# Kernel tuning notes

Measured on AMD Instinct MI355X. Metric: run time of the kernel, lower is better.

Reference implementation:

```python
import jax, jax.numpy as jnp
import numpy as np

EPS = 1e-5

def masked_group_norm(x, mask, gamma, beta, num_groups):
    # x: [B,D,H,W,C] (zero at unoccupied), mask: [B,D,H,W,1] float
    B, D, H, W, C = x.shape
    G = num_groups
    Cg = C // G
    xg = x.reshape(B, -1, G, Cg)          # [B,V,G,Cg]
    m = mask.reshape(B, -1, 1, 1)         # [B,V,1,1]
    cnt = jnp.maximum(m.sum(axis=1, keepdims=True) * Cg, 1.0)  # elems per (B,G)
    mean = (xg * m).sum(axis=(1, 3), keepdims=True) / cnt
    var = (((xg - mean) ** 2) * m).sum(axis=(1, 3), keepdims=True) / cnt
    y = (xg - mean) * jax.lax.rsqrt(var + EPS)
    y = y.reshape(B, D, H, W, C)
    return (y * gamma + beta) * mask

def downsample2(x, mask):
    # mean-pool occupied children under coords//2; new site occupied if any child is
    B, D, H, W, C = x.shape
    xr = x.reshape(B, D // 2, 2, H // 2, 2, W // 2, 2, C)
    mr = mask.reshape(B, D // 2, 2, H // 2, 2, W // 2, 2, 1)
    cnt = mr.sum(axis=(2, 4, 6))
    y = xr.sum(axis=(2, 4, 6)) / jnp.maximum(cnt, 1.0)
    new_mask = (cnt > 0).astype(x.dtype)
    return y, new_mask

def subm_conv3d(x, w, b, mask):
    # submanifold conv: unoccupied inputs are zero; outputs only at occupied sites
    y = jax.lax.conv_general_dilated(
        x, w, window_strides=(1, 1, 1), padding='SAME',
        dimension_numbers=('NDHWC', 'DHWIO', 'NDHWC'))
    return (y + b) * mask

def setup_inputs() -> dict:
    key = jax.random.key(0)
    ks = jax.random.split(key, 12)
    B, D, C, Co = 4, 64, 64, 128
    x = jax.random.normal(ks[0], (B, D, D, D, C), dtype=jnp.float32)
    mask = jax.random.randint(ks[1], (B, D, D, D), 0, 2).astype(jnp.int32)
    s = 0.05
    return {
        'x': x, 'mask': mask,
        'gn1_w': jnp.ones((C,), jnp.float32), 'gn1_b': jnp.zeros((C,), jnp.float32),
        'w1': jax.random.normal(ks[2], (3, 3, 3, C, Co), jnp.float32) * s,
        'b1': jax.random.normal(ks[3], (Co,), jnp.float32) * s,
        'gn2_w': jnp.ones((Co,), jnp.float32), 'gn2_b': jnp.zeros((Co,), jnp.float32),
        'w2': jax.random.normal(ks[4], (3, 3, 3, Co, Co), jnp.float32) * s,
        'b2': jax.random.normal(ks[5], (Co,), jnp.float32) * s,
        'wskip': jax.random.normal(ks[6], (C, Co), jnp.float32) * s,
        'bskip': jax.random.normal(ks[7], (Co,), jnp.float32) * s,
    }

def reference(x, mask, gn1_w, gn1_b, w1, b1, gn2_w, gn2_b, w2, b2, wskip, bskip):
    NUM_GROUPS = 32
    m = mask.astype(x.dtype)[..., None]          # [B,D,H,W,1]
    x = x * m                                    # sparse tensor: zero off-mask
    # act_layers: SparseGroupNorm32 + SparseSiLU
    h = masked_group_norm(x, m, gn1_w, gn1_b, NUM_GROUPS)
    h = jax.nn.silu(h)                           # silu(0)=0, stays sparse
    # downsample both h and residual x
    h, dm = downsample2(h, m)
    xd, _ = downsample2(x, m)
    # out_layers: conv3 -> GN -> SiLU -> conv3
    h = subm_conv3d(h, w1, b1, dm)
    h = masked_group_norm(h, dm, gn2_w, gn2_b, NUM_GROUPS)
    h = jax.nn.silu(h)
    h = subm_conv3d(h, w2, b2, dm)
    # skip: 1x1 sparse conv (out_channels != channels)
    skip = (jnp.einsum('bdhwc,co->bdhwo', xd, wskip) + bskip) * dm
    return h + skip
```

## Files before the change

kernel.cpp:

```cpp
#include <hip/hip_runtime.h>
#include <cstdint>
#include <cstddef>

#define B_ 4
#define V1 262144
#define C1 64
#define V2 32768
#define C2 128
#define TOTV 131072
#define P_ 34
#define P2_ 1156
#define P3_ 39304
#define SBSTRIDE ((size_t)4 * P3_)

#define OFF_S1A 0
#define OFF_S2A 128
#define OFF_CNT1 256
#define OFF_S1B 260
#define OFF_S2B 388
#define OFF_CNT2 516

typedef __bf16 bf16x8 __attribute__((ext_vector_type(8)));
typedef float f32x4 __attribute__((ext_vector_type(4)));

__device__ __forceinline__ float bf2f(unsigned short u) {
    return __builtin_bit_cast(float, (unsigned)u << 16);
}
__device__ __forceinline__ unsigned short f2bf(float f) {
    unsigned u = __builtin_bit_cast(unsigned, f);
    u += 0x7fffu + ((u >> 16) & 1u);
    return (unsigned short)(u >> 16);
}
__device__ __forceinline__ float fast_silu(float x) {
    return x * __builtin_amdgcn_rcpf(1.f + __expf(-x));
}

__device__ __forceinline__ int a_ofs(int ks, int csh) {
    int s = ks & ((1 << csh) - 1), tap = ks >> csh;
    int dz = tap / 9, r = tap % 9, dy = r / 3, dx = r % 3;
    return s * (int)(SBSTRIDE * 64) + (dz * P2_ + dy * P_ + dx) * 64;
}

__global__ __launch_bounds__(256) void k0z_prep(const float* __restrict__ w1,
                                                const float* __restrict__ w2,
                                                const float* __restrict__ wskip,
                                                unsigned short* __restrict__ w1t,
                                                unsigned short* __restrict__ w2t,
                                                int* __restrict__ d1,
                                                int* __restrict__ d2,
                                                unsigned short* __restrict__ h1p,
                                                unsigned short* __restrict__ h2p)
{
    if (blockIdx.x >= 2624) {
        int i = (blockIdx.x - 2624) * 256 + threadIdx.x;
        if (i >= 24 * P3_) return;
        int sb = i / P3_, vox = i % P3_;
        int vz = vox / P2_, r = vox % P2_, vy = r / P_, vx = r % P_;
        bool border = (vz == 0) | (vz == 33) | (vy == 0) | (vy == 33) | (vx == 0) | (vx == 33);
        if (!border) return;
        unsigned short* base = (sb < 8) ? (h1p + (size_t)sb * P3_ * 32 + (size_t)vox * 32)
                                        : (h2p + (size_t)(sb - 8) * P3_ * 32 + (size_t)vox * 32);
        uint4 z = {0, 0, 0, 0};
        uint4* b4 = (uint4*)base;
        b4[0] = z; b4[1] = z; b4[2] = z; b4[3] = z;
        return;
    }
    int i = blockIdx.x * 256 + threadIdx.x;
    if (blockIdx.x == 0) {
        int t = threadIdx.x;
        if (t < 54)               d1[t] = (t + 1 < 54)  ? a_ofs(t + 1, 1) - a_ofs(t, 1) : 0;
        if (t >= 64 && t < 172) { int j = t - 64;
                                  d2[j] = (j + 1 < 108) ? a_ofs(j + 1, 2) - a_ofs(j, 2) : 0; }
    }
    if (i < 54 * 4096) {
        int slab = i >> 12, r = i & 4095;
        int q = r >> 10, n = (r >> 3) & 127, j = r & 7;
        int t = slab >> 1, s = slab & 1;
        int ci = s * 32 + q * 8 + j;
        w1t[i] = f2bf(w1[((size_t)t * 64 + ci) * 128 + n]);
    }
    int i2 = i - 54 * 4096;
    if (i2 >= 0 && i2 < 110 * 4096) {
        int slab = i2 >> 12, r = i2 & 4095;
        int q = r >> 10, n = (r >> 3) & 127, j = r & 7;
        float v;
        if (slab < 108) {
            int t = slab >> 2, s = slab & 3;
            int ci = s * 32 + q * 8 + j;
            v = w2[((size_t)t * 128 + ci) * 128 + n];
        } else {
            int ci = (slab - 108) * 32 + q * 8 + j;
            v = wskip[(size_t)ci * 128 + n];
        }
        w2t[i2] = f2bf(v);
    }
}

__global__ __launch_bounds__(256) void k1_stats1(const float* __restrict__ x,
                                                 const int* __restrict__ mask,
                                                 float* __restrict__ stats)
{
    __shared__ float ls1[32], ls2[32];
    __shared__ float lcnt;
    int tid = threadIdx.x;
    if (tid < 32) { ls1[tid] = 0.f; ls2[tid] = 0.f; }
    if (tid == 0) lcnt = 0.f;
    __syncthreads();

    int b  = blockIdx.x & 3;
    int bb = blockIdx.x >> 2;
    int c4 = tid & 15;
    int vl = tid >> 4;

    const float* xb = x + ((size_t)b * V1) * C1;
    const int*   mb = mask + (size_t)b * V1;

    float s1a = 0.f, s2a = 0.f, s1b = 0.f, s2b = 0.f, mc = 0.f;
    for (int ch = bb; ch < V1 / 16; ch += 1024) {
        int v = ch * 16 + vl;
        int m = mb[v];
        if (c4 == 0) mc += (float)m;
        if (m) {
            float4 xv = *(const float4*)(xb + (size_t)v * C1 + c4 * 4);
            s1a += xv.x + xv.y;  s2a += xv.x * xv.x + xv.y * xv.y;
            s1b += xv.z + xv.w;  s2b += xv.z * xv.z + xv.w * xv.w;
        }
    }
    atomicAdd(&ls1[2 * c4],     s1a); atomicAdd(&ls2[2 * c4],     s2a);
    atomicAdd(&ls1[2 * c4 + 1], s1b); atomicAdd(&ls2[2 * c4 + 1], s2b);
    if (c4 == 0) atomicAdd(&lcnt, mc);
    __syncthreads();
    if (tid < 32) {
        atomicAdd(&stats[OFF_S1A + b * 32 + tid], ls1[tid]);
        atomicAdd(&stats[OFF_S2A + b * 32 + tid], ls2[tid]);
    }
    if (tid == 0) atomicAdd(&stats[OFF_CNT1 + b], lcnt);
}

__global__ __launch_bounds__(256) void k2_down(const float* __restrict__ x,
                                               const int* __restrict__ mask,
                                               const float* __restrict__ gn1w,
                                               const float* __restrict__ gn1b,
                                               float* __restrict__ stats,
                                               unsigned short* __restrict__ h1p,
                                               unsigned short* __restrict__ xdb,
                                               float* __restrict__ dm)
{
    __shared__ float bcnt;
    int tid = threadIdx.x;
    if (tid == 0) bcnt = 0.f;
    __syncthreads();
    int c  = tid & 63;
    int vl = tid >> 6;
    const size_t ovbase = (size_t)blockIdx.x * 32;
    const int b = (int)(ovbase >> 15);

    int g = c >> 1;
    float ce   = fmaxf(stats[OFF_CNT1 + b] * 2.f, 1.f);
    float mean = stats[OFF_S1A + b * 32 + g] / ce;
    float var  = stats[OFF_S2A + b * 32 + g] / ce - mean * mean;
    float rinv = rsqrtf(var + 1e-5f);
    float a  = rinv * gn1w[c];
    float bc = gn1b[c] - mean * a;

    const int*   mb = mask + ((size_t)b << 18);
    const float* xb = x + (((size_t)b << 18) << 6);

    float mycnt = 0.f;
    #pragma unroll 2
    for (int it = 0; it < 8; ++it) {
        size_t ov = ovbase + it * 4 + vl;
        int v2 = (int)(ov & 32767);
        int z = v2 >> 10, y = (v2 >> 5) & 31, xk = v2 & 31;

        float hacc = 0.f, xacc = 0.f; int cnt = 0;
        #pragma unroll
        for (int dz = 0; dz < 2; ++dz)
        #pragma unroll
        for (int dy = 0; dy < 2; ++dy)
        #pragma unroll
        for (int dx = 0; dx < 2; ++dx) {
            int v1 = ((2 * z + dz) << 12) | ((2 * y + dy) << 6) | (2 * xk + dx);
            if (mb[v1]) {
                cnt++;
                float xv = xb[(size_t)v1 * 64 + c];
                xacc += xv;
                hacc += fast_silu(fmaf(xv, a, bc));
            }
        }
        float inv = __builtin_amdgcn_rcpf(fmaxf((float)cnt, 1.f));
        int pvox = (z + 1) * P2_ + (y + 1) * P_ + (xk + 1);
        size_t so = ((size_t)(c >> 5) * SBSTRIDE + (size_t)b * P3_ + pvox) * 32 + (c & 31);
        h1p[so] = f2bf(hacc * inv);
        xdb[ov * 64 + c] = f2bf(xacc * inv);
        if (c == 0) {
            float d = (cnt > 0) ? 1.f : 0.f;
            dm[ov] = d;
            mycnt += d;
        }
    }
    if (c == 0) atomicAdd(&bcnt, mycnt);
    __syncthreads();
    if (tid == 0) atomicAdd(&stats[OFF_CNT2 + b], bcnt);
}

template<int CIN, bool SKIP>
__global__ __launch_bounds__(256, 2) void conv3_mfma(
    const unsigned short* __restrict__ srcP,
    const unsigned short* __restrict__ sksrc,
    const unsigned short* __restrict__ wT,
    const int* __restrict__ tblA,
    const float* __restrict__ bias,
    const float* __restrict__ bias2,
    const float* __restrict__ dm,
    float* __restrict__ outf,
    unsigned short* __restrict__ outb,
    float* __restrict__ statsOut)
{
    constexpr int CS   = CIN / 32;
    constexpr int NKM  = 27 * CS;
    constexpr int NPHM = NKM / 2;
    constexpr int NPH  = NPHM + (SKIP ? 1 : 0);

    __shared__ short smem[2][8192];

    const int tid  = threadIdx.x;
    const int lane = tid & 63;
    const int wv   = tid >> 6;
    const int orig = blockIdx.x;
    const int blk  = (orig & 7) * 64 + (orig >> 3);
    const int b    = blk >> 7;
    const int z    = (blk >> 2) & 31;
    const int yo   = blk & 3;
    const int y0   = yo * 8 + wv * 2;
    const int vb   = b * 32768;
    const int klo  = (lane >> 4) * 8;
    const int xl   = lane & 15;
    const int rlo  = (lane >> 4) * 4;

    f32x4 acc[4][8];
    #pragma unroll
    for (int f = 0; f < 4; ++f)
        #pragma unroll
        for (int nb = 0; nb < 8; ++nb)
            acc[f][nb] = (f32x4){0.f, 0.f, 0.f, 0.f};

    const char* pA = (const char*)srcP +
        (((size_t)b * P3_ + (size_t)(z * P2_ + y0 * P_ + xl)) * 32 + klo) * 2;

    auto loadSkip = [&](int ss, bf16x8* af) {
        const unsigned short* abase = sksrc + ss * 32;
        #pragma unroll
        for (int fy = 0; fy < 2; ++fy)
            #pragma unroll
            for (int fx = 0; fx < 2; ++fx)
                af[fy * 2 + fx] = *(const bf16x8*)(abase +
                    (size_t)(vb + z * 1024 + (y0 + fy) * 32 + fx * 16 + xl) * 64 + klo);
    };

    auto stageW = [&](int pr, int buf) {
        const char* g = (const char*)wT + (size_t)pr * 16384 + wv * 1024 + (lane << 4);
        char* l = (char*)&smem[0][0] + buf * 16384 + wv * 1024;
        #pragma unroll
        for (int j = 0; j < 4; ++j)
            __builtin_amdgcn_global_load_lds(
                (const __attribute__((address_space(1))) unsigned int*)(g + j * 4096),
                (__attribute__((address_space(3))) unsigned int*)(l + j * 4096),
                16, 0, 0);
    };

    auto loadAStep = [&](int ks, bf16x8* af) {
        af[0] = *(const bf16x8*)pA;
        af[1] = *(const bf16x8*)(pA + 1024);
        af[2] = *(const bf16x8*)(pA + 2176);
        af[3] = *(const bf16x8*)(pA + 3200);
        pA += tblA[ks];
    };

    bf16x8 afc[8];
    stageW(0, 0);
    loadAStep(0, &afc[0]);
    loadAStep(1, &afc[4]);
    asm volatile("s_waitcnt vmcnt(8)" ::: "memory");
    __builtin_amdgcn_s_barrier();

    int cur = 0;
    #pragma unroll 2
    for (int p = 0; p < NPH; ++p) {
        const bool more = (p + 1 < NPH);
        bf16x8 afn[8] = {{}, {}, {}, {}, {}, {}, {}, {}};
        if (more) {
            stageW(p + 1, cur ^ 1);
            if (2 * p + 2 < NKM) {
                loadAStep(2 * p + 2, &afn[0]);
                loadAStep(2 * p + 3, &afn[4]);
            } else if (SKIP) {
                loadSkip(0, &afn[0]);
                loadSkip(1, &afn[4]);
            }
        }
        __builtin_amdgcn_s_setprio(1);
        #pragma unroll
        for (int ss = 0; ss < 2; ++ss) {
            const short* bp = &smem[0][0] + cur * 8192 + ss * 4096 +
                              ((lane >> 4) * 128 + xl) * 8;
            #pragma unroll
            for (int nb = 0; nb < 8; ++nb) {
                bf16x8 bfr = *(const bf16x8*)(bp + nb * 128);
                acc[0][nb] = __builtin_amdgcn_mfma_f32_16x16x32_bf16(afc[ss * 4 + 0], bfr, acc[0][nb], 0, 0, 0);
                acc[1][nb] = __builtin_amdgcn_mfma_f32_16x16x32_bf16(afc[ss * 4 + 1], bfr, acc[1][nb], 0, 0, 0);
                acc[2][nb] = __builtin_amdgcn_mfma_f32_16x16x32_bf16(afc[ss * 4 + 2], bfr, acc[2][nb], 0, 0, 0);
                acc[3][nb] = __builtin_amdgcn_mfma_f32_16x16x32_bf16(afc[ss * 4 + 3], bfr, acc[3][nb], 0, 0, 0);
            }
        }
        __builtin_amdgcn_s_setprio(0);
        if (more) asm volatile("s_waitcnt vmcnt(8)" ::: "memory");
        else      asm volatile("s_waitcnt vmcnt(0)" ::: "memory");
        asm volatile("s_waitcnt lgkmcnt(0)" ::: "memory");
        __builtin_amdgcn_s_barrier();
        #pragma unroll
        for (int j = 0; j < 8; ++j) afc[j] = afn[j];
        cur ^= 1;
    }

    float bv[8];
    #pragma unroll
    for (int nb = 0; nb < 8; ++nb) {
        int co = nb * 16 + xl;
        if constexpr (SKIP) bv[nb] = bias[co] + bias2[co];
        else                bv[nb] = bias[co];
    }
    if constexpr (SKIP) {
        #pragma unroll
        for (int f = 0; f < 4; ++f) {
            const int fy = f >> 1, fx = f & 1;
            const int vox0 = vb + z * 1024 + (y0 + fy) * 32 + fx * 16 + rlo;
            float4 dm4 = *(const float4*)(dm + vox0);
            #pragma unroll
            for (int j = 0; j < 4; ++j) {
                const float dmx = (j == 0) ? dm4.x : (j == 1) ? dm4.y : (j == 2) ? dm4.z : dm4.w;
                const size_t obase = (size_t)(vox0 + j) * 128 + xl;
                #pragma unroll
                for (int nb = 0; nb < 8; ++nb) {
                    float o = (acc[f][nb][j] + bv[nb]) * dmx;
                    outf[obase + nb * 16] = o;
                }
            }
        }
    } else {
        float ps1[8], ps2[8];
        #pragma unroll
        for (int nb = 0; nb < 8; ++nb) { ps1[nb] = 0.f; ps2[nb] = 0.f; }
        #pragma unroll
        for (int f = 0; f < 4; ++f) {
            const int fy = f >> 1, fx = f & 1;
            const int yrow = y0 + fy;
            const int xc0  = fx * 16 + rlo;
            const int vox0 = vb + z * 1024 + yrow * 32 + xc0;
            float4 dm4 = *(const float4*)(dm + vox0);
            #pragma unroll
            for (int j = 0; j < 4; ++j) {
                const float dmx = (j == 0) ? dm4.x : (j == 1) ? dm4.y : (j == 2) ? dm4.z : dm4.w;
                const int pvox = (z + 1) * P2_ + (yrow + 1) * P_ + (xc0 + j + 1);
                const size_t sbase = (size_t)b * P3_ + pvox;
                #pragma unroll
                for (int nb = 0; nb < 8; ++nb) {
                    float o = (acc[f][nb][j] + bv[nb]) * dmx;
                    int co = nb * 16 + xl;
                    size_t so = ((size_t)(co >> 5) * SBSTRIDE + sbase) * 32 + (co & 31);
                    outb[so] = f2bf(o);
                    ps1[nb] += o; ps2[nb] += o * o;
                }
            }
        }
        float* lsum = (float*)&smem[0][0];
        __syncthreads();
        if (tid < 64) lsum[tid] = 0.f;
        __syncthreads();
        #pragma unroll
        for (int nb = 0; nb < 8; ++nb) {
            float s1 = ps1[nb], s2 = ps2[nb];
            s1 += __shfl_xor(s1, 1);  s2 += __shfl_xor(s2, 1);
            s1 += __shfl_xor(s1, 2);  s2 += __shfl_xor(s2, 2);
            s1 += __shfl_xor(s1, 16); s2 += __shfl_xor(s2, 16);
            s1 += __shfl_xor(s1, 32); s2 += __shfl_xor(s2, 32);
            if ((lane & 0x33) == 0) {
                int g = nb * 4 + (xl >> 2);
                atomicAdd(&lsum[g], s1);
                atomicAdd(&lsum[32 + g], s2);
            }
        }
        __syncthreads();
        if (tid < 32) {
            atomicAdd(&statsOut[OFF_S1B + b * 32 + tid], lsum[tid]);
            atomicAdd(&statsOut[OFF_S2B + b * 32 + tid], lsum[32 + tid]);
        }
    }
}

__global__ __launch_bounds__(256) void k5_gn2(unsigned short* __restrict__ h2p,
                                              const float* __restrict__ stats,
                                              const float* __restrict__ dm,
                                              const float* __restrict__ gn2w,
                                              const float* __restrict__ gn2b)
{
    int tid = threadIdx.x;
    int g = tid & 31;
    const int idx0 = blockIdx.x * 2048;
    const int b = (idx0 >> 5) >> 15;

    float ce   = fmaxf(stats[OFF_CNT2 + b] * 4.f, 1.f);
    float mean = stats[OFF_S1B + b * 32 + g] / ce;
    float var  = stats[OFF_S2B + b * 32 + g] / ce - mean * mean;
    float rinv = rsqrtf(var + 1e-5f);
    float4 gw = *(const float4*)(gn2w + g * 4);
    float4 gb = *(const float4*)(gn2b + g * 4);
    float ax = rinv * gw.x, bx = gb.x - mean * ax;
    float ay = rinv * gw.y, by = gb.y - mean * ay;
    float az = rinv * gw.z, bz = gb.z - mean * az;
    float aw = rinv * gw.w, bw = gb.w - mean * aw;

    #pragma unroll 2
    for (int it = 0; it < 8; ++it) {
        int idx = idx0 + it * 256 + tid;
        int v = idx >> 5;
        int v2 = v & 32767;
        float dmv = dm[v];
        int zz = v2 >> 10, yy = (v2 >> 5) & 31, xx = v2 & 31;
        int pvox = (zz + 1) * P2_ + (yy + 1) * P_ + (xx + 1);
        size_t so = ((size_t)(g >> 3) * SBSTRIDE + (size_t)b * P3_ + pvox) * 32 + (g & 7) * 4;
        ushort4 hv = *(const ushort4*)(h2p + so);
        float t;
        ushort4 o;
        t = fmaf(bf2f(hv.x), ax, bx) * dmv; o.x = f2bf(fast_silu(t));
        t = fmaf(bf2f(hv.y), ay, by) * dmv; o.y = f2bf(fast_silu(t));
        t = fmaf(bf2f(hv.z), az, bz) * dmv; o.z = f2bf(fast_silu(t));
        t = fmaf(bf2f(hv.w), aw, bw) * dmv; o.w = f2bf(fast_silu(t));
        *(ushort4*)(h2p + so) = o;
    }
}

extern "C" void kernel_launch(void* const* d_in, const int* in_sizes, int n_in,
                              void* d_out, int out_size, void* d_ws, size_t ws_size,
                              hipStream_t stream)
{
    const float* x     = (const float*)d_in[0];
    const int*   mask  = (const int*)d_in[1];
    const float* gn1w  = (const float*)d_in[2];
    const float* gn1b  = (const float*)d_in[3];
    const float* w1    = (const float*)d_in[4];
    const float* b1    = (const float*)d_in[5];
    const float* gn2w  = (const float*)d_in[6];
    const float* gn2b  = (const float*)d_in[7];
    const float* w2    = (const float*)d_in[8];
    const float* b2    = (const float*)d_in[9];
    const float* wskip = (const float*)d_in[10];
    const float* bskip = (const float*)d_in[11];
    float* out = (float*)d_out;

    char* wsb = (char*)d_ws;
    float*          stats = (float*)wsb;
    float*          dm    = (float*)(wsb + 4096);
    unsigned short* h1p   = (unsigned short*)(wsb + 528384);
    unsigned short* xdb   = (unsigned short*)(wsb + 20652032);
    unsigned short* h2p   = (unsigned short*)(wsb + 70983680);
    unsigned short* w1t   = (unsigned short*)(wsb + 111230976);
    unsigned short* w2t   = (unsigned short*)(wsb + 111673344);
    int*            d1    = (int*)(wsb + 112574464);
    int*            d2    = (int*)(wsb + 112574720);

    hipMemsetAsync(stats, 0, 520 * sizeof(float), stream);

    hipLaunchKernelGGL(k0z_prep, dim3(2624 + 3685), dim3(256), 0, stream,
                       w1, w2, wskip, w1t, w2t, d1, d2, h1p, h2p);
    hipLaunchKernelGGL(k1_stats1, dim3(4096), dim3(256), 0, stream, x, mask, stats);
    hipLaunchKernelGGL(k2_down, dim3(4096), dim3(256), 0, stream,
                       x, mask, gn1w, gn1b, stats, h1p, xdb, dm);
    hipLaunchKernelGGL((conv3_mfma<64, false>), dim3(512), dim3(256), 0, stream,
                       h1p, (const unsigned short*)nullptr, w1t, d1, b1, (const float*)nullptr,
                       dm, (float*)nullptr, h2p, stats);
    hipLaunchKernelGGL(k5_gn2, dim3(2048), dim3(256), 0, stream, h2p, stats, dm, gn2w, gn2b);
    hipLaunchKernelGGL((conv3_mfma<128, true>), dim3(512), dim3(256), 0, stream,
                       h2p, xdb, w2t, d2, b2, bskip, dm, out, (unsigned short*)nullptr,
                       (float*)nullptr);
}
```

Baseline: 374.4 us.

## Split conv output channels across wave pairs and merge prep with stats kernel

The conv kernel now splits each block's work 2x2 across waves: two waves cover y rows and two cover halves of the 128 output channels. This halves the accumulators per wave, allows 3 blocks per CU, and doubles the grid to 1024 blocks so more CUs are occupied, at the cost of each wave loading A fragments for only half the channels (more redundant A traffic). Separately, the weight/border prep kernel is merged into the stats1 kernel to remove one launch.

```diff
diff --git a/kernel.cpp b/kernel.cpp
--- a/kernel.cpp
+++ b/kernel.cpp
@@ -41,68 +41,70 @@
     return s * (int)(SBSTRIDE * 64) + (dz * P2_ + dy * P_ + dx) * 64;
 }
 
-__global__ __launch_bounds__(256) void k0z_prep(const float* __restrict__ w1,
-                                                const float* __restrict__ w2,
-                                                const float* __restrict__ wskip,
-                                                unsigned short* __restrict__ w1t,
-                                                unsigned short* __restrict__ w2t,
-                                                int* __restrict__ d1,
-                                                int* __restrict__ d2,
-                                                unsigned short* __restrict__ h1p,
-                                                unsigned short* __restrict__ h2p)
+__global__ __launch_bounds__(256) void k01_stats_prep(const float* __restrict__ x,
+                                                      const int* __restrict__ mask,
+                                                      float* __restrict__ stats,
+                                                      const float* __restrict__ w1,
+                                                      const float* __restrict__ w2,
+                                                      const float* __restrict__ wskip,
+                                                      unsigned short* __restrict__ w1t,
+                                                      unsigned short* __restrict__ w2t,
+                                                      int* __restrict__ d1,
+                                                      int* __restrict__ d2,
+                                                      unsigned short* __restrict__ h1p,
+                                                      unsigned short* __restrict__ h2p)
 {
-    if (blockIdx.x >= 2624) {
-        int i = (blockIdx.x - 2624) * 256 + threadIdx.x;
-        if (i >= 24 * P3_) return;
-        int sb = i / P3_, vox = i % P3_;
-        int vz = vox / P2_, r = vox % P2_, vy = r / P_, vx = r % P_;
-        bool border = (vz == 0) | (vz == 33) | (vy == 0) | (vy == 33) | (vx == 0) | (vx == 33);
-        if (!border) return;
-        unsigned short* base = (sb < 8) ? (h1p + (size_t)sb * P3_ * 32 + (size_t)vox * 32)
-                                        : (h2p + (size_t)(sb - 8) * P3_ * 32 + (size_t)vox * 32);
-        uint4 z = {0, 0, 0, 0};
-        uint4* b4 = (uint4*)base;
-        b4[0] = z; b4[1] = z; b4[2] = z; b4[3] = z;
+    int tid = threadIdx.x;
+    if (blockIdx.x >= 4096) {
+        int pb = blockIdx.x - 4096;
+        if (pb >= 2624) {
+            int i = (pb - 2624) * 256 + tid;
+            if (i >= 24 * P3_) return;
+            int sb = i / P3_, vox = i % P3_;
+            int vz = vox / P2_, r = vox % P2_, vy = r / P_, vx = r % P_;
+            bool border = (vz == 0) | (vz == 33) | (vy == 0) | (vy == 33) | (vx == 0) | (vx == 33);
+            if (!border) return;
+            unsigned short* base = (sb < 8) ? (h1p + (size_t)sb * P3_ * 32 + (size_t)vox * 32)
+                                            : (h2p + (size_t)(sb - 8) * P3_ * 32 + (size_t)vox * 32);
+            uint4 z = {0, 0, 0, 0};
+            uint4* b4 = (uint4*)base;
+            b4[0] = z; b4[1] = z; b4[2] = z; b4[3] = z;
+            return;
+        }
+        int i = pb * 256 + tid;
+        if (pb == 0) {
+            int t = tid;
+            if (t < 54)               d1[t] = (t + 1 < 54)  ? a_ofs(t + 1, 1) - a_ofs(t, 1) : 0;
+            if (t >= 64 && t < 172) { int j = t - 64;
+                                      d2[j] = (j + 1 < 108) ? a_ofs(j + 1, 2) - a_ofs(j, 2) : 0; }
+        }
+        if (i < 54 * 4096) {
+            int slab = i >> 12, r = i & 4095;
+            int q = r >> 10, n = (r >> 3) & 127, j = r & 7;
+            int t = slab >> 1, s = slab & 1;
+            int ci = s * 32 + q * 8 + j;
+            w1t[i] = f2bf(w1[((size_t)t * 64 + ci) * 128 + n]);
+        }
+        int i2 = i - 54 * 4096;
+        if (i2 >= 0 && i2 < 110 * 4096) {
+            int slab = i2 >> 12, r = i2 & 4095;
+            int q = r >> 10, n = (r >> 3) & 127, j = r & 7;
+            float v;
+            if (slab < 108) {
+                int t = slab >> 2, s = slab & 3;
+                int ci = s * 32 + q * 8 + j;
+                v = w2[((size_t)t * 128 + ci) * 128 + n];
+            } else {
+                int ci = (slab - 108) * 32 + q * 8 + j;
+                v = wskip[(size_t)ci * 128 + n];
+            }
+            w2t[i2] = f2bf(v);
+        }
         return;
     }
-    int i = blockIdx.x * 256 + threadIdx.x;
-    if (blockIdx.x == 0) {
-        int t = threadIdx.x;
-        if (t < 54)               d1[t] = (t + 1 < 54)  ? a_ofs(t + 1, 1) - a_ofs(t, 1) : 0;
-        if (t >= 64 && t < 172) { int j = t - 64;
-                                  d2[j] = (j + 1 < 108) ? a_ofs(j + 1, 2) - a_ofs(j, 2) : 0; }
-    }
-    if (i < 54 * 4096) {
-        int slab = i >> 12, r = i & 4095;
-        int q = r >> 10, n = (r >> 3) & 127, j = r & 7;
-        int t = slab >> 1, s = slab & 1;
-        int ci = s * 32 + q * 8 + j;
-        w1t[i] = f2bf(w1[((size_t)t * 64 + ci) * 128 + n]);
-    }
-    int i2 = i - 54 * 4096;
-    if (i2 >= 0 && i2 < 110 * 4096) {
-        int slab = i2 >> 12, r = i2 & 4095;
-        int q = r >> 10, n = (r >> 3) & 127, j = r & 7;
-        float v;
-        if (slab < 108) {
-            int t = slab >> 2, s = slab & 3;
-            int ci = s * 32 + q * 8 + j;
-            v = w2[((size_t)t * 128 + ci) * 128 + n];
-        } else {
-            int ci = (slab - 108) * 32 + q * 8 + j;
-            v = wskip[(size_t)ci * 128 + n];
-        }
-        w2t[i2] = f2bf(v);
-    }
-}
-
-__global__ __launch_bounds__(256) void k1_stats1(const float* __restrict__ x,
-                                                 const int* __restrict__ mask,
-                                                 float* __restrict__ stats)
-{
+
     __shared__ float ls1[32], ls2[32];
     __shared__ float lcnt;
-    int tid = threadIdx.x;
     if (tid < 32) { ls1[tid] = 0.f; ls2[tid] = 0.f; }
     if (tid == 0) lcnt = 0.f;
     __syncthreads();
@@ -205,7 +207,7 @@
 }
 
 template<int CIN, bool SKIP>
-__global__ __launch_bounds__(256, 2) void conv3_mfma(
+__global__ __launch_bounds__(256, 3) void conv3_mfma(
     const unsigned short* __restrict__ srcP,
     const unsigned short* __restrict__ sksrc,
     const unsigned short* __restrict__ wT,
@@ -227,22 +229,24 @@
     const int tid  = threadIdx.x;
     const int lane = tid & 63;
     const int wv   = tid >> 6;
+    const int wm   = wv >> 1;
+    const int wn   = wv & 1;
     const int orig = blockIdx.x;
-    const int blk  = (orig & 7) * 64 + (orig >> 3);
-    const int b    = blk >> 7;
-    const int z    = (blk >> 2) & 31;
-    const int yo   = blk & 3;
-    const int y0   = yo * 8 + wv * 2;
+    const int blk  = (orig & 7) * 128 + (orig >> 3);
+    const int b    = blk >> 8;
+    const int z    = (blk >> 3) & 31;
+    const int yo   = blk & 7;
+    const int y0   = yo * 4 + wm * 2;
     const int vb   = b * 32768;
     const int klo  = (lane >> 4) * 8;
     const int xl   = lane & 15;
     const int rlo  = (lane >> 4) * 4;
 
-    f32x4 acc[4][8];
+    f32x4 acc[4][4];
     #pragma unroll
     for (int f = 0; f < 4; ++f)
         #pragma unroll
-        for (int nb = 0; nb < 8; ++nb)
+        for (int nb = 0; nb < 4; ++nb)
             acc[f][nb] = (f32x4){0.f, 0.f, 0.f, 0.f};
 
     const char* pA = (const char*)srcP +
@@ -303,9 +307,9 @@
         #pragma unroll
         for (int ss = 0; ss < 2; ++ss) {
             const short* bp = &smem[0][0] + cur * 8192 + ss * 4096 +
-                              ((lane >> 4) * 128 + xl) * 8;
+                              (lane >> 4) * 1024 + (wn * 64 + xl) * 8;
             #pragma unroll
-            for (int nb = 0; nb < 8; ++nb) {
+            for (int nb = 0; nb < 4; ++nb) {
                 bf16x8 bfr = *(const bf16x8*)(bp + nb * 128);
                 acc[0][nb] = __builtin_amdgcn_mfma_f32_16x16x32_bf16(afc[ss * 4 + 0], bfr, acc[0][nb], 0, 0, 0);
                 acc[1][nb] = __builtin_amdgcn_mfma_f32_16x16x32_bf16(afc[ss * 4 + 1], bfr, acc[1][nb], 0, 0, 0);
@@ -323,10 +327,10 @@
         cur ^= 1;
     }
 
-    float bv[8];
+    float bv[4];
     #pragma unroll
-    for (int nb = 0; nb < 8; ++nb) {
-        int co = nb * 16 + xl;
+    for (int nb = 0; nb < 4; ++nb) {
+        int co = wn * 64 + nb * 16 + xl;
         if constexpr (SKIP) bv[nb] = bias[co] + bias2[co];
         else                bv[nb] = bias[co];
     }
@@ -339,18 +343,18 @@
             #pragma unroll
             for (int j = 0; j < 4; ++j) {
                 const float dmx = (j == 0) ? dm4.x : (j == 1) ? dm4.y : (j == 2) ? dm4.z : dm4.w;
-                const size_t obase = (size_t)(vox0 + j) * 128 + xl;
+                const size_t obase = (size_t)(vox0 + j) * 128 + wn * 64 + xl;
                 #pragma unroll
-                for (int nb = 0; nb < 8; ++nb) {
+                for (int nb = 0; nb < 4; ++nb) {
                     float o = (acc[f][nb][j] + bv[nb]) * dmx;
                     outf[obase + nb * 16] = o;
                 }
             }
         }
     } else {
-        float ps1[8], ps2[8];
-        #pragma unroll
-        for (int nb = 0; nb < 8; ++nb) { ps1[nb] = 0.f; ps2[nb] = 0.f; }
+        float ps1[4], ps2[4];
+        #pragma unroll
+        for (int nb = 0; nb < 4; ++nb) { ps1[nb] = 0.f; ps2[nb] = 0.f; }
         #pragma unroll
         for (int f = 0; f < 4; ++f) {
             const int fy = f >> 1, fx = f & 1;
@@ -364,9 +368,9 @@
                 const int pvox = (z + 1) * P2_ + (yrow + 1) * P_ + (xc0 + j + 1);
                 const size_t sbase = (size_t)b * P3_ + pvox;
                 #pragma unroll
-                for (int nb = 0; nb < 8; ++nb) {
+                for (int nb = 0; nb < 4; ++nb) {
                     float o = (acc[f][nb][j] + bv[nb]) * dmx;
-                    int co = nb * 16 + xl;
+                    int co = wn * 64 + nb * 16 + xl;
                     size_t so = ((size_t)(co >> 5) * SBSTRIDE + sbase) * 32 + (co & 31);
                     outb[so] = f2bf(o);
                     ps1[nb] += o; ps2[nb] += o * o;
@@ -378,14 +382,14 @@
         if (tid < 64) lsum[tid] = 0.f;
         __syncthreads();
         #pragma unroll
-        for (int nb = 0; nb < 8; ++nb) {
+        for (int nb = 0; nb < 4; ++nb) {
             float s1 = ps1[nb], s2 = ps2[nb];
             s1 += __shfl_xor(s1, 1);  s2 += __shfl_xor(s2, 1);
             s1 += __shfl_xor(s1, 2);  s2 += __shfl_xor(s2, 2);
             s1 += __shfl_xor(s1, 16); s2 += __shfl_xor(s2, 16);
             s1 += __shfl_xor(s1, 32); s2 += __shfl_xor(s2, 32);
             if ((lane & 0x33) == 0) {
-                int g = nb * 4 + (xl >> 2);
+                int g = wn * 16 + nb * 4 + (xl >> 2);
                 atomicAdd(&lsum[g], s1);
                 atomicAdd(&lsum[32 + g], s2);
             }
@@ -471,16 +475,15 @@
 
     hipMemsetAsync(stats, 0, 520 * sizeof(float), stream);
 
-    hipLaunchKernelGGL(k0z_prep, dim3(2624 + 3685), dim3(256), 0, stream,
-                       w1, w2, wskip, w1t, w2t, d1, d2, h1p, h2p);
-    hipLaunchKernelGGL(k1_stats1, dim3(4096), dim3(256), 0, stream, x, mask, stats);
+    hipLaunchKernelGGL(k01_stats_prep, dim3(4096 + 2624 + 3685), dim3(256), 0, stream,
+                       x, mask, stats, w1, w2, wskip, w1t, w2t, d1, d2, h1p, h2p);
     hipLaunchKernelGGL(k2_down, dim3(4096), dim3(256), 0, stream,
                        x, mask, gn1w, gn1b, stats, h1p, xdb, dm);
-    hipLaunchKernelGGL((conv3_mfma<64, false>), dim3(512), dim3(256), 0, stream,
+    hipLaunchKernelGGL((conv3_mfma<64, false>), dim3(1024), dim3(256), 0, stream,
                        h1p, (const unsigned short*)nullptr, w1t, d1, b1, (const float*)nullptr,
                        dm, (float*)nullptr, h2p, stats);
     hipLaunchKernelGGL(k5_gn2, dim3(2048), dim3(256), 0, stream, h2p, stats, dm, gn2w, gn2b);
-    hipLaunchKernelGGL((conv3_mfma<128, true>), dim3(512), dim3(256), 0, stream,
+    hipLaunchKernelGGL((conv3_mfma<128, true>), dim3(1024), dim3(256), 0, stream,
                        h2p, xdb, w2t, d2, b2, bskip, dm, out, (unsigned short*)nullptr,
                        (float*)nullptr);
 }
```

New measurement: 417.9 us. 11.6% more time.
